# Optimization experiments

Measured on AMD Instinct MI355X. Metric: run time of the kernel, lower is better.

Reference implementation:

```python
import jax, jax.numpy as jnp
import numpy as np

N, E = 20000, 320000
H = 4            # heads per layer
C_IN, C_HID, C_OUT = 128, 64, 64
NEG_SLOPE = 0.2  # PyG GATConv default leaky_relu slope


def setup_inputs() -> dict:
    key = jax.random.key(0)
    ks = jax.random.split(key, 16)
    p = lambda k, shape: jax.random.normal(k, shape, jnp.float32) * 0.1
    return {
        "x": jax.random.normal(ks[0], (N, C_IN), jnp.float32),
        "edge_index": jax.random.randint(ks[1], (2, E), 0, N),
        # layer 0: in C_IN -> H*C_HID (concat)
        "W0": p(ks[2], (C_IN, H * C_HID)),
        "as0": p(ks[3], (H, C_HID)),
        "ad0": p(ks[4], (H, C_HID)),
        "b0": jnp.zeros((H * C_HID,), jnp.float32),
        # layer 1: in H*C_HID -> H*C_HID (concat)
        "W1": p(ks[5], (H * C_HID, H * C_HID)),
        "as1": p(ks[6], (H, C_HID)),
        "ad1": p(ks[7], (H, C_HID)),
        "b1": jnp.zeros((H * C_HID,), jnp.float32),
        # output layer: in H*C_HID -> C_OUT (mean over heads, concat=False)
        "W2": p(ks[8], (H * C_HID, H * C_OUT)),
        "as2": p(ks[9], (H, C_OUT)),
        "ad2": p(ks[10], (H, C_OUT)),
        "b2": jnp.zeros((C_OUT,), jnp.float32),
    }


def _gat_layer(x, src, dst, W, a_src, a_dst, b, concat):
    """PyG GATConv (eval mode): gather -> edge attention -> segment softmax -> scatter."""
    n = x.shape[0]
    h = (x @ W).reshape(n, H, -1)                      # [N, H, C]
    e_src = (h * a_src).sum(-1)                        # [N, H]
    e_dst = (h * a_dst).sum(-1)                        # [N, H]
    logits = jax.nn.leaky_relu(e_src[src] + e_dst[dst], NEG_SLOPE)   # [E', H]
    m = jax.lax.stop_gradient(jax.ops.segment_max(logits, dst, num_segments=n))
    ex = jnp.exp(logits - m[dst])
    denom = jax.ops.segment_sum(ex, dst, num_segments=n)
    alpha = ex / denom[dst]                            # [E', H] segment softmax per dst node
    out = jax.ops.segment_sum(h[src] * alpha[:, :, None], dst, num_segments=n)  # [N, H, C]
    out = out.reshape(n, -1) if concat else out.mean(axis=1)
    return out + b, alpha


def reference(x, edge_index, W0, as0, ad0, b0, W1, as1, ad1, b1, W2, as2, ad2, b2):
    n = x.shape[0]
    loops = jnp.arange(n, dtype=edge_index.dtype)      # GATConv adds self-loops
    src = jnp.concatenate([edge_index[0], loops])
    dst = jnp.concatenate([edge_index[1], loops])
    h, a0 = _gat_layer(x, src, dst, W0, as0, ad0, b0, True)
    h = jax.nn.elu(h)
    h, a1 = _gat_layer(h, src, dst, W1, as1, ad1, b1, True)
    h = jax.nn.elu(h)
    out, a2 = _gat_layer(h, src, dst, W2, as2, ad2, b2, False)
    return out, a0, a1, a2
```

## Files before the change

kernel.cpp:

```cpp
#include <hip/hip_runtime.h>
#include <hip/hip_bf16.h>
#include <math.h>

#define HCOLS 256
#define NHEAD 4
#define CDIM  64
#define NEG_SLOPE 0.2f

typedef __attribute__((ext_vector_type(8))) short bf16x8;
typedef __attribute__((ext_vector_type(4))) float f32x4;

__device__ __forceinline__ float leaky(float v) { return v > 0.f ? v : v * NEG_SLOPE; }
__device__ __forceinline__ unsigned short f2bf(float f) {
    unsigned u = __float_as_uint(f);
    u += 0x7fff + ((u >> 16) & 1);
    return (unsigned short)(u >> 16);
}

__device__ __forceinline__ void fma8(float* acc, uint4 hv, float a) {
    acc[0] = fmaf(a, __uint_as_float(hv.x << 16),          acc[0]);
    acc[1] = fmaf(a, __uint_as_float(hv.x & 0xffff0000u),  acc[1]);
    acc[2] = fmaf(a, __uint_as_float(hv.y << 16),          acc[2]);
    acc[3] = fmaf(a, __uint_as_float(hv.y & 0xffff0000u),  acc[3]);
    acc[4] = fmaf(a, __uint_as_float(hv.z << 16),          acc[4]);
    acc[5] = fmaf(a, __uint_as_float(hv.z & 0xffff0000u),  acc[5]);
    acc[6] = fmaf(a, __uint_as_float(hv.w << 16),          acc[6]);
    acc[7] = fmaf(a, __uint_as_float(hv.w & 0xffff0000u),  acc[7]);
}

__global__ void zero_deg_kernel(int* __restrict__ deg, int n) {
    int i = blockIdx.x * 256 + threadIdx.x;
    if (i < n) deg[i] = 0;
}

__global__ void deg_kernel(const int* __restrict__ ei, int* __restrict__ deg,
                           int E, int Ep) {
    int e = blockIdx.x * 256 + threadIdx.x;
    if (e >= Ep) return;
    int d = (e < E) ? ei[E + e] : (e - E);
    atomicAdd(&deg[d], 1);
}

__global__ void scan_kernel(const int* __restrict__ deg, int* __restrict__ rowptr,
                            int* __restrict__ cursor, int n) {
    __shared__ int wsum[16];
    int tid = threadIdx.x;
    int lane = tid & 63, w = tid >> 6;
    int CH = (n + 1023) >> 10;
    int base = tid * CH;
    int s = 0;
    for (int k = 0; k < CH; ++k) {
        int i = base + k;
        s += (i < n) ? deg[i] : 0;
    }
    int incl = s;
#pragma unroll
    for (int d = 1; d < 64; d <<= 1) {
        int t = __shfl_up(incl, d, 64);
        if (lane >= d) incl += t;
    }
    if (lane == 63) wsum[w] = incl;
    __syncthreads();
    if (w == 0) {
        int v = (lane < 16) ? wsum[lane] : 0;
#pragma unroll
        for (int d = 1; d < 16; d <<= 1) {
            int t = __shfl_up(v, d, 64);
            if (lane >= d) v += t;
        }
        if (lane < 16) wsum[lane] = v;
    }
    __syncthreads();
    int woff = (w == 0) ? 0 : wsum[w - 1];
    int run = woff + incl - s;
    for (int k = 0; k < CH; ++k) {
        int i = base + k;
        if (i < n) { rowptr[i] = run; cursor[i] = run; run += deg[i]; }
    }
    if (tid == 1023) rowptr[n] = run;
}

__global__ void fill_kernel(const int* __restrict__ ei, int* __restrict__ cursor,
                            int* __restrict__ eidx, int E, int Ep) {
    int e = blockIdx.x * 256 + threadIdx.x;
    if (e >= Ep) return;
    int d = (e < E) ? ei[E + e] : (e - E);
    int pos = atomicAdd(&cursor[d], 1);
    eidx[pos] = e;
}

__global__ void wconv_kernel(const float* __restrict__ W0, const float* __restrict__ W1,
                             const float* __restrict__ W2,
                             unsigned short* __restrict__ Wt0, unsigned short* __restrict__ Wt1,
                             unsigned short* __restrict__ Wt2) {
    __shared__ float t[32][33];
    int z = blockIdx.z;
    const float* W = (z == 0) ? W0 : (z == 1) ? W1 : W2;
    unsigned short* Wt = (z == 0) ? Wt0 : (z == 1) ? Wt1 : Wt2;
    int K = (z == 0) ? 128 : 256;
    if (blockIdx.y * 32 >= K) return;
    int bx = blockIdx.x;
    int by = blockIdx.y;
    int tx = threadIdx.x & 31, ty = threadIdx.x >> 5;
#pragma unroll
    for (int i = 0; i < 32; i += 8)
        t[ty + i][tx] = W[(by * 32 + ty + i) * HCOLS + bx * 32 + tx];
    __syncthreads();
#pragma unroll
    for (int i = 0; i < 32; i += 8)
        Wt[(size_t)(bx * 32 + ty + i) * K + by * 32 + tx] = f2bf(t[tx][ty + i]);
}

template <int K, bool SRC_F32>
__global__ void gemm_kernel(const void* __restrict__ Xv, const unsigned short* __restrict__ Wt,
                            unsigned short* __restrict__ Hout,
                            const float* __restrict__ As, const float* __restrict__ Ad,
                            float* __restrict__ esrc, float* __restrict__ edst,
                            int n) {
    constexpr int LDK = K + 16;
    __shared__ __align__(16) unsigned short a_sh[32 * LDK];
    int row0 = blockIdx.x * 32;
    int tid = threadIdx.x;

    constexpr int CH = 32 * K / 8;
    for (int c = tid; c < CH; c += 256) {
        int r = c / (K / 8), kc = c % (K / 8);
        int row = row0 + r;
        uint4 pack;
        if (row < n) {
            if (SRC_F32) {
                const float* X = (const float*)Xv;
                float4 f0 = *reinterpret_cast<const float4*>(&X[(size_t)row * K + kc * 8]);
                float4 f1 = *reinterpret_cast<const float4*>(&X[(size_t)row * K + kc * 8 + 4]);
                pack.x = f2bf(f0.x) | ((unsigned)f2bf(f0.y) << 16);
                pack.y = f2bf(f0.z) | ((unsigned)f2bf(f0.w) << 16);
                pack.z = f2bf(f1.x) | ((unsigned)f2bf(f1.y) << 16);
                pack.w = f2bf(f1.z) | ((unsigned)f2bf(f1.w) << 16);
            } else {
                const uint4* X = (const uint4*)Xv;
                pack = X[((size_t)row * K + kc * 8) / 8];
            }
        } else {
            pack = make_uint4(0, 0, 0, 0);
        }
        *reinterpret_cast<uint4*>(&a_sh[r * LDK + kc * 8]) = pack;
    }
    __syncthreads();

    int lane = tid & 63;
    int w = tid >> 6;
    int lr = lane & 15;
    int lk = (lane >> 4) * 8;

    f32x4 acc[2][4];
#pragma unroll
    for (int m = 0; m < 2; ++m)
#pragma unroll
        for (int nf = 0; nf < 4; ++nf) acc[m][nf] = (f32x4){0.f, 0.f, 0.f, 0.f};

    const unsigned short* wt = Wt + (size_t)(w * 64) * K;
#pragma unroll
    for (int ks = 0; ks < K / 32; ++ks) {
        bf16x8 a[2], b[4];
#pragma unroll
        for (int m = 0; m < 2; ++m)
            a[m] = *reinterpret_cast<const bf16x8*>(&a_sh[(16 * m + lr) * LDK + ks * 32 + lk]);
#pragma unroll
        for (int nf = 0; nf < 4; ++nf)
            b[nf] = *reinterpret_cast<const bf16x8*>(&wt[(size_t)(16 * nf + lr) * K + ks * 32 + lk]);
#pragma unroll
        for (int m = 0; m < 2; ++m)
#pragma unroll
            for (int nf = 0; nf < 4; ++nf)
                acc[m][nf] = __builtin_amdgcn_mfma_f32_16x16x32_bf16(a[m], b[nf], acc[m][nf], 0, 0, 0);
    }

    float as_v[4], ad_v[4];
#pragma unroll
    for (int nf = 0; nf < 4; ++nf) {
        as_v[nf] = As[w * 64 + 16 * nf + lr];
        ad_v[nf] = Ad[w * 64 + 16 * nf + lr];
    }
#pragma unroll
    for (int m = 0; m < 2; ++m) {
#pragma unroll
        for (int j = 0; j < 4; ++j) {
            int row_g = row0 + 16 * m + (lane >> 4) * 4 + j;
            bool ok = row_g < n;
#pragma unroll
            for (int nf = 0; nf < 4; ++nf) {
                if (ok) Hout[(size_t)row_g * HCOLS + w * 64 + 16 * nf + lr] = f2bf(acc[m][nf][j]);
            }
            float ps = acc[m][0][j] * as_v[0] + acc[m][1][j] * as_v[1] +
                       acc[m][2][j] * as_v[2] + acc[m][3][j] * as_v[3];
            float pd = acc[m][0][j] * ad_v[0] + acc[m][1][j] * ad_v[1] +
                       acc[m][2][j] * ad_v[2] + acc[m][3][j] * ad_v[3];
#pragma unroll
            for (int off = 1; off < 16; off <<= 1) {
                ps += __shfl_xor(ps, off, 64);
                pd += __shfl_xor(pd, off, 64);
            }
            if (lr == 0 && ok) {
                esrc[row_g * NHEAD + w] = ps;
                edst[row_g * NHEAD + w] = pd;
            }
        }
    }
}

template <int MODE>
__launch_bounds__(256, 4)
__global__ void attn_agg_kernel(const unsigned short* __restrict__ h,
                                const float* __restrict__ esrc,
                                const float* __restrict__ edst,
                                const int* __restrict__ ei,
                                const int* __restrict__ rowptr,
                                const int* __restrict__ eidx,
                                const float* __restrict__ bias,
                                float* __restrict__ alpha,
                                void* __restrict__ xout,
                                int n, int E) {
    __shared__ __align__(16) float aT[16][64][NHEAD];
    __shared__ int sArr[16][64];

    int tid = threadIdx.x;
    int wave = tid >> 6, lane = tid & 63;
    int g = lane >> 4, t = lane & 15;
    int nodeblk = blockIdx.x * 16;
    int nidx = wave * 4 + g;
    int node = nodeblk + nidx;
    bool gvalid = node < n;
    int s0 = 0, s1 = 0;
    if (gvalid) { s0 = rowptr[node]; s1 = rowptr[node + 1]; }
    int deg = s1 - s0;
    float4 ed = make_float4(0.f, 0.f, 0.f, 0.f);
    if (gvalid) ed = *reinterpret_cast<const float4*>(&edst[node * NHEAD]);

    const float NEGINF = -3.4e38f;
    float4 lgc[4]; int sc[4], ec[4];
    int degc = deg < 64 ? deg : 64;
    int nch = (degc + 15) >> 4;
    float4 mx = make_float4(NEGINF, NEGINF, NEGINF, NEGINF);
#pragma unroll
    for (int c = 0; c < 4; ++c) {
        sc[c] = 0; ec[c] = 0;
        lgc[c] = make_float4(NEGINF, NEGINF, NEGINF, NEGINF);
        if (c < nch) {
            int i = s0 + c * 16 + t;
            bool v = i < s1;
            int e = v ? eidx[i] : 0;
            int s = v ? ((e < E) ? ei[e] : (e - E)) : 0;
            sc[c] = s; ec[c] = e;
            if (v) {
                float4 es = *reinterpret_cast<const float4*>(&esrc[s * NHEAD]);
                lgc[c].x = leaky(es.x + ed.x);
                lgc[c].y = leaky(es.y + ed.y);
                lgc[c].z = leaky(es.z + ed.z);
                lgc[c].w = leaky(es.w + ed.w);
            }
            mx.x = fmaxf(mx.x, lgc[c].x);
            mx.y = fmaxf(mx.y, lgc[c].y);
            mx.z = fmaxf(mx.z, lgc[c].z);
            mx.w = fmaxf(mx.w, lgc[c].w);
        }
    }
    for (int i = s0 + 64 + t; i < s1; i += 16) {
        int e = eidx[i];
        int s = (e < E) ? ei[e] : (e - E);
        float4 es = *reinterpret_cast<const float4*>(&esrc[s * NHEAD]);
        mx.x = fmaxf(mx.x, leaky(es.x + ed.x));
        mx.y = fmaxf(mx.y, leaky(es.y + ed.y));
        mx.z = fmaxf(mx.z, leaky(es.z + ed.z));
        mx.w = fmaxf(mx.w, leaky(es.w + ed.w));
    }
#pragma unroll
    for (int off = 1; off < 16; off <<= 1) {
        mx.x = fmaxf(mx.x, __shfl_xor(mx.x, off, 64));
        mx.y = fmaxf(mx.y, __shfl_xor(mx.y, off, 64));
        mx.z = fmaxf(mx.z, __shfl_xor(mx.z, off, 64));
        mx.w = fmaxf(mx.w, __shfl_xor(mx.w, off, 64));
    }
    float4 exc[4];
    float4 sm = make_float4(0.f, 0.f, 0.f, 0.f);
#pragma unroll
    for (int c = 0; c < 4; ++c) {
        exc[c] = make_float4(0.f, 0.f, 0.f, 0.f);
        if (c < nch) {
            exc[c].x = __expf(lgc[c].x - mx.x);
            exc[c].y = __expf(lgc[c].y - mx.y);
            exc[c].z = __expf(lgc[c].z - mx.z);
            exc[c].w = __expf(lgc[c].w - mx.w);
            sm.x += exc[c].x; sm.y += exc[c].y; sm.z += exc[c].z; sm.w += exc[c].w;
        }
    }
    for (int i = s0 + 64 + t; i < s1; i += 16) {
        int e = eidx[i];
        int s = (e < E) ? ei[e] : (e - E);
        float4 es = *reinterpret_cast<const float4*>(&esrc[s * NHEAD]);
        sm.x += __expf(leaky(es.x + ed.x) - mx.x);
        sm.y += __expf(leaky(es.y + ed.y) - mx.y);
        sm.z += __expf(leaky(es.z + ed.z) - mx.z);
        sm.w += __expf(leaky(es.w + ed.w) - mx.w);
    }
#pragma unroll
    for (int off = 1; off < 16; off <<= 1) {
        sm.x += __shfl_xor(sm.x, off, 64);
        sm.y += __shfl_xor(sm.y, off, 64);
        sm.z += __shfl_xor(sm.z, off, 64);
        sm.w += __shfl_xor(sm.w, off, 64);
    }
    float4 inv = make_float4(1.f / sm.x, 1.f / sm.y, 1.f / sm.z, 1.f / sm.w);
#pragma unroll
    for (int c = 0; c < 4; ++c) {
        if (c < nch) {
            float4 al4;
            al4.x = exc[c].x * inv.x; al4.y = exc[c].y * inv.y;
            al4.z = exc[c].z * inv.z; al4.w = exc[c].w * inv.w;
            int i = s0 + c * 16 + t;
            if (i < s1) *reinterpret_cast<float4*>(&alpha[(size_t)ec[c] * NHEAD]) = al4;
            *reinterpret_cast<float4*>(&aT[nidx][c * 16 + t][0]) = al4;
            sArr[nidx][c * 16 + t] = sc[c];
        }
    }
    for (int i = s0 + 64 + t; i < s1; i += 16) {
        int e = eidx[i];
        int s = (e < E) ? ei[e] : (e - E);
        float4 es = *reinterpret_cast<const float4*>(&esrc[s * NHEAD]);
        float4 av;
        av.x = __expf(leaky(es.x + ed.x) - mx.x) * inv.x;
        av.y = __expf(leaky(es.y + ed.y) - mx.y) * inv.y;
        av.z = __expf(leaky(es.z + ed.z) - mx.z) * inv.z;
        av.w = __expf(leaky(es.w + ed.w) - mx.w) * inv.w;
        *reinterpret_cast<float4*>(&alpha[(size_t)e * NHEAD]) = av;
    }
    if (__any(deg > 64)) __threadfence();

    asm volatile("s_waitcnt lgkmcnt(0)" ::: "memory");
    __builtin_amdgcn_sched_barrier(0);

    int half = lane >> 5;
    int q = lane & 31;
    int head = q >> 3;
    unsigned byteoff = (unsigned)q * 16u;
    const char* hb = (const char*)h;

    for (int g2 = 0; g2 < 4; ++g2) {
        int nd = nodeblk + wave * 4 + g2;
        if (nd >= n) break;
        int t0 = rowptr[nd], t1 = rowptr[nd + 1];
        int dg = t1 - t0;
        int m = dg < 64 ? dg : 64;
        int m2 = (m + 1) & ~1;
        const float* ap = &aT[wave * 4 + g2][0][0] + head;
        const int* sp = &sArr[wave * 4 + g2][0];
        float acc[8];
#pragma unroll
        for (int k = 0; k < 8; ++k) acc[k] = 0.f;
        int j = 0;
        for (; j + 4 <= m2; j += 4) {
            int jA = j + half, jB = j + 2 + half;
            int sA = sp[jA], sB = sp[jB];
            float aA = ap[jA * NHEAD], aB = ap[jB * NHEAD];
            uint4 hA = *reinterpret_cast<const uint4*>(hb + (((unsigned)sA) << 9) + byteoff);
            uint4 hB = *reinterpret_cast<const uint4*>(hb + (((unsigned)sB) << 9) + byteoff);
            fma8(acc, hA, aA);
            fma8(acc, hB, aB);
        }
        for (; j < m2; j += 2) {
            int jA = j + half;
            int sA = sp[jA];
            float aA = ap[jA * NHEAD];
            uint4 hA = *reinterpret_cast<const uint4*>(hb + (((unsigned)sA) << 9) + byteoff);
            fma8(acc, hA, aA);
        }
        if (dg > 64) {
            for (int i = t0 + 64; i < t1; ++i) {
                if (half == 0) {
                    int e = eidx[i];
                    int s = (e < E) ? ei[e] : (e - E);
                    float a = alpha[(size_t)e * NHEAD + head];
                    uint4 hv = *reinterpret_cast<const uint4*>(hb + (((unsigned)s) << 9) + byteoff);
                    fma8(acc, hv, a);
                }
            }
        }
#pragma unroll
        for (int k = 0; k < 8; ++k) acc[k] += __shfl_xor(acc[k], 32, 64);

        if (MODE == 0) {
            if (half == 0) {
                float4 b0 = *reinterpret_cast<const float4*>(&bias[q * 8]);
                float4 b1 = *reinterpret_cast<const float4*>(&bias[q * 8 + 4]);
                float v0 = acc[0] + b0.x, v1 = acc[1] + b0.y, v2 = acc[2] + b0.z, v3 = acc[3] + b0.w;
                float v4 = acc[4] + b1.x, v5 = acc[5] + b1.y, v6 = acc[6] + b1.z, v7 = acc[7] + b1.w;
                v0 = v0 > 0.f ? v0 : expm1f(v0);
                v1 = v1 > 0.f ? v1 : expm1f(v1);
                v2 = v2 > 0.f ? v2 : expm1f(v2);
                v3 = v3 > 0.f ? v3 : expm1f(v3);
                v4 = v4 > 0.f ? v4 : expm1f(v4);
                v5 = v5 > 0.f ? v5 : expm1f(v5);
                v6 = v6 > 0.f ? v6 : expm1f(v6);
                v7 = v7 > 0.f ? v7 : expm1f(v7);
                uint4 o;
                o.x = (unsigned)f2bf(v0) | ((unsigned)f2bf(v1) << 16);
                o.y = (unsigned)f2bf(v2) | ((unsigned)f2bf(v3) << 16);
                o.z = (unsigned)f2bf(v4) | ((unsigned)f2bf(v5) << 16);
                o.w = (unsigned)f2bf(v6) | ((unsigned)f2bf(v7) << 16);
                *reinterpret_cast<uint4*>(&((unsigned short*)xout)[(size_t)nd * HCOLS + q * 8]) = o;
            }
        } else {
#pragma unroll
            for (int k = 0; k < 8; ++k) {
                acc[k] += __shfl_xor(acc[k], 8, 64);
                acc[k] += __shfl_xor(acc[k], 16, 64);
            }
            if (half == 0 && q < 8) {
                float* op = (float*)xout + (size_t)nd * CDIM + q * 8;
                float4 r0, r1;
                r0.x = acc[0] * 0.25f + bias[q * 8 + 0];
                r0.y = acc[1] * 0.25f + bias[q * 8 + 1];
                r0.z = acc[2] * 0.25f + bias[q * 8 + 2];
                r0.w = acc[3] * 0.25f + bias[q * 8 + 3];
                r1.x = acc[4] * 0.25f + bias[q * 8 + 4];
                r1.y = acc[5] * 0.25f + bias[q * 8 + 5];
                r1.z = acc[6] * 0.25f + bias[q * 8 + 6];
                r1.w = acc[7] * 0.25f + bias[q * 8 + 7];
                *reinterpret_cast<float4*>(op) = r0;
                *reinterpret_cast<float4*>(op + 4) = r1;
            }
        }
    }
}

extern "C" void kernel_launch(void* const* d_in, const int* in_sizes, int n_in,
                              void* d_out, int out_size, void* d_ws, size_t ws_size,
                              hipStream_t stream) {
    const float* x   = (const float*)d_in[0];
    const int*   ei  = (const int*)d_in[1];
    const float* W0  = (const float*)d_in[2];
    const float* as0 = (const float*)d_in[3];
    const float* ad0 = (const float*)d_in[4];
    const float* b0  = (const float*)d_in[5];
    const float* W1  = (const float*)d_in[6];
    const float* as1 = (const float*)d_in[7];
    const float* ad1 = (const float*)d_in[8];
    const float* b1  = (const float*)d_in[9];
    const float* W2  = (const float*)d_in[10];
    const float* as2 = (const float*)d_in[11];
    const float* ad2 = (const float*)d_in[12];
    const float* b2  = (const float*)d_in[13];

    const int N  = in_sizes[0] / 128;
    const int E  = in_sizes[1] / 2;
    const int Ep = E + N;

    float* out = (float*)d_out;
    float* a0  = out + (size_t)N * CDIM;
    float* a1  = a0 + (size_t)Ep * NHEAD;
    float* a2  = a1 + (size_t)Ep * NHEAD;

    char* wp = (char*)d_ws;
    auto carve = [&](size_t bytes) {
        char* p = wp;
        wp += (bytes + 255) & ~(size_t)255;
        return (void*)p;
    };
    unsigned short* hbuf = (unsigned short*)carve((size_t)N * HCOLS * 2);
    unsigned short* xbuf = (unsigned short*)carve((size_t)N * HCOLS * 2);
    float* esrc   = (float*)carve((size_t)N * NHEAD * 4);
    float* edst   = (float*)carve((size_t)N * NHEAD * 4);
    int*   deg    = (int*)carve((size_t)N * 4);
    int*   rowptr = (int*)carve((size_t)(N + 1) * 4);
    int*   cursor = (int*)carve((size_t)N * 4);
    int*   eidx   = (int*)carve((size_t)Ep * 4);
    unsigned short* Wt0 = (unsigned short*)carve((size_t)HCOLS * 128 * 2);
    unsigned short* Wt1 = (unsigned short*)carve((size_t)HCOLS * HCOLS * 2);
    unsigned short* Wt2 = (unsigned short*)carve((size_t)HCOLS * HCOLS * 2);

    zero_deg_kernel<<<(N + 255) / 256, 256, 0, stream>>>(deg, N);
    deg_kernel<<<(Ep + 255) / 256, 256, 0, stream>>>(ei, deg, E, Ep);
    scan_kernel<<<1, 1024, 0, stream>>>(deg, rowptr, cursor, N);
    fill_kernel<<<(Ep + 255) / 256, 256, 0, stream>>>(ei, cursor, eidx, E, Ep);

    wconv_kernel<<<dim3(8, 8, 3), 256, 0, stream>>>(W0, W1, W2, Wt0, Wt1, Wt2);

    int gemm_grid = (N + 31) / 32;
    int agg_grid  = (N + 15) / 16;

    gemm_kernel<128, true><<<gemm_grid, 256, 0, stream>>>(x, Wt0, hbuf, as0, ad0, esrc, edst, N);
    attn_agg_kernel<0><<<agg_grid, 256, 0, stream>>>(hbuf, esrc, edst, ei, rowptr, eidx, b0, a0, xbuf, N, E);

    gemm_kernel<256, false><<<gemm_grid, 256, 0, stream>>>(xbuf, Wt1, hbuf, as1, ad1, esrc, edst, N);
    attn_agg_kernel<0><<<agg_grid, 256, 0, stream>>>(hbuf, esrc, edst, ei, rowptr, eidx, b1, a1, xbuf, N, E);

    gemm_kernel<256, false><<<gemm_grid, 256, 0, stream>>>(xbuf, Wt2, hbuf, as2, ad2, esrc, edst, N);
    attn_agg_kernel<1><<<agg_grid, 256, 0, stream>>>(hbuf, esrc, edst, ei, rowptr, eidx, b2, a2, out, N, E);
}
```

Baseline: 233.5 us.

## Restructure aggregation to per-head edge-parallel loop and fuse prep kernels

The aggregation phase now loops over heads, with each wave lane group handling 8 edges in parallel per head (8 lanes covering a head's 64 channels). The shared alpha tile is stored head-major, and concat-mode outputs are staged in shared memory before a coalesced bias+ELU write. This is meant to raise memory-level parallelism on the gathered neighbor rows, at the cost of more cross-lane shuffle reductions and an extra shared buffer. Separately, the degree zeroing and weight transpose/convert kernels are merged into one launch to save a kernel launch.

```diff
diff --git a/kernel.cpp b/kernel.cpp
--- a/kernel.cpp
+++ b/kernel.cpp
@@ -28,9 +28,34 @@
     acc[7] = fmaf(a, __uint_as_float(hv.w & 0xffff0000u),  acc[7]);
 }
 
-__global__ void zero_deg_kernel(int* __restrict__ deg, int n) {
-    int i = blockIdx.x * 256 + threadIdx.x;
-    if (i < n) deg[i] = 0;
+__global__ void prep_kernel(const float* __restrict__ W0, const float* __restrict__ W1,
+                            const float* __restrict__ W2,
+                            unsigned short* __restrict__ Wt0, unsigned short* __restrict__ Wt1,
+                            unsigned short* __restrict__ Wt2,
+                            int* __restrict__ deg, int n, int nzb) {
+    int b = blockIdx.x;
+    if (b < nzb) {
+        int i = b * 256 + threadIdx.x;
+        if (i < n) deg[i] = 0;
+        return;
+    }
+    b -= nzb;
+    int z = b >> 6;
+    int rem = b & 63;
+    int bx = rem & 7, by = rem >> 3;
+    const float* W = (z == 0) ? W0 : (z == 1) ? W1 : W2;
+    unsigned short* Wt = (z == 0) ? Wt0 : (z == 1) ? Wt1 : Wt2;
+    int K = (z == 0) ? 128 : 256;
+    if (by * 32 >= K) return;
+    __shared__ float t[32][33];
+    int tx = threadIdx.x & 31, ty = threadIdx.x >> 5;
+#pragma unroll
+    for (int i = 0; i < 32; i += 8)
+        t[ty + i][tx] = W[(by * 32 + ty + i) * HCOLS + bx * 32 + tx];
+    __syncthreads();
+#pragma unroll
+    for (int i = 0; i < 32; i += 8)
+        Wt[(size_t)(bx * 32 + ty + i) * K + by * 32 + tx] = f2bf(t[tx][ty + i]);
 }
 
 __global__ void deg_kernel(const int* __restrict__ ei, int* __restrict__ deg,
@@ -87,28 +112,6 @@
     int d = (e < E) ? ei[E + e] : (e - E);
     int pos = atomicAdd(&cursor[d], 1);
     eidx[pos] = e;
-}
-
-__global__ void wconv_kernel(const float* __restrict__ W0, const float* __restrict__ W1,
-                             const float* __restrict__ W2,
-                             unsigned short* __restrict__ Wt0, unsigned short* __restrict__ Wt1,
-                             unsigned short* __restrict__ Wt2) {
-    __shared__ float t[32][33];
-    int z = blockIdx.z;
-    const float* W = (z == 0) ? W0 : (z == 1) ? W1 : W2;
-    unsigned short* Wt = (z == 0) ? Wt0 : (z == 1) ? Wt1 : Wt2;
-    int K = (z == 0) ? 128 : 256;
-    if (blockIdx.y * 32 >= K) return;
-    int bx = blockIdx.x;
-    int by = blockIdx.y;
-    int tx = threadIdx.x & 31, ty = threadIdx.x >> 5;
-#pragma unroll
-    for (int i = 0; i < 32; i += 8)
-        t[ty + i][tx] = W[(by * 32 + ty + i) * HCOLS + bx * 32 + tx];
-    __syncthreads();
-#pragma unroll
-    for (int i = 0; i < 32; i += 8)
-        Wt[(size_t)(bx * 32 + ty + i) * K + by * 32 + tx] = f2bf(t[tx][ty + i]);
 }
 
 template <int K, bool SRC_F32>
@@ -220,8 +223,9 @@
                                 float* __restrict__ alpha,
                                 void* __restrict__ xout,
                                 int n, int E) {
-    __shared__ __align__(16) float aT[16][64][NHEAD];
+    __shared__ __align__(16) float aTh[16][NHEAD][72];
     __shared__ int sArr[16][64];
+    __shared__ __align__(16) float outbuf[MODE == 0 ? 16 : 1][MODE == 0 ? 256 : 4];
 
     int tid = threadIdx.x;
     int wave = tid >> 6, lane = tid & 63;
@@ -318,8 +322,12 @@
             al4.z = exc[c].z * inv.z; al4.w = exc[c].w * inv.w;
             int i = s0 + c * 16 + t;
             if (i < s1) *reinterpret_cast<float4*>(&alpha[(size_t)ec[c] * NHEAD]) = al4;
-            *reinterpret_cast<float4*>(&aT[nidx][c * 16 + t][0]) = al4;
-            sArr[nidx][c * 16 + t] = sc[c];
+            int eo = c * 16 + t;
+            aTh[nidx][0][eo] = al4.x;
+            aTh[nidx][1][eo] = al4.y;
+            aTh[nidx][2][eo] = al4.z;
+            aTh[nidx][3][eo] = al4.w;
+            sArr[nidx][eo] = sc[c];
         }
     }
     for (int i = s0 + 64 + t; i < s1; i += 16) {
@@ -338,94 +346,116 @@
     asm volatile("s_waitcnt lgkmcnt(0)" ::: "memory");
     __builtin_amdgcn_sched_barrier(0);
 
-    int half = lane >> 5;
-    int q = lane & 31;
-    int head = q >> 3;
-    unsigned byteoff = (unsigned)q * 16u;
+    int ed8 = lane >> 3;
+    int ch  = lane & 7;
     const char* hb = (const char*)h;
-
+    unsigned chb = (unsigned)(ch * 16);
+
+    int t0r[4], t1r[4];
+#pragma unroll
     for (int g2 = 0; g2 < 4; ++g2) {
         int nd = nodeblk + wave * 4 + g2;
-        if (nd >= n) break;
-        int t0 = rowptr[nd], t1 = rowptr[nd + 1];
-        int dg = t1 - t0;
-        int m = dg < 64 ? dg : 64;
-        int m2 = (m + 1) & ~1;
-        const float* ap = &aT[wave * 4 + g2][0][0] + head;
-        const int* sp = &sArr[wave * 4 + g2][0];
-        float acc[8];
-#pragma unroll
-        for (int k = 0; k < 8; ++k) acc[k] = 0.f;
-        int j = 0;
-        for (; j + 4 <= m2; j += 4) {
-            int jA = j + half, jB = j + 2 + half;
-            int sA = sp[jA], sB = sp[jB];
-            float aA = ap[jA * NHEAD], aB = ap[jB * NHEAD];
-            uint4 hA = *reinterpret_cast<const uint4*>(hb + (((unsigned)sA) << 9) + byteoff);
-            uint4 hB = *reinterpret_cast<const uint4*>(hb + (((unsigned)sB) << 9) + byteoff);
-            fma8(acc, hA, aA);
-            fma8(acc, hB, aB);
-        }
-        for (; j < m2; j += 2) {
-            int jA = j + half;
-            int sA = sp[jA];
-            float aA = ap[jA * NHEAD];
-            uint4 hA = *reinterpret_cast<const uint4*>(hb + (((unsigned)sA) << 9) + byteoff);
-            fma8(acc, hA, aA);
-        }
-        if (dg > 64) {
-            for (int i = t0 + 64; i < t1; ++i) {
-                if (half == 0) {
-                    int e = eidx[i];
-                    int s = (e < E) ? ei[e] : (e - E);
-                    float a = alpha[(size_t)e * NHEAD + head];
-                    uint4 hv = *reinterpret_cast<const uint4*>(hb + (((unsigned)s) << 9) + byteoff);
-                    fma8(acc, hv, a);
+        t0r[g2] = 0; t1r[g2] = 0;
+        if (nd < n) { t0r[g2] = rowptr[nd]; t1r[g2] = rowptr[nd + 1]; }
+    }
+
+    float macc[4][8];
+    if (MODE == 1) {
+#pragma unroll
+        for (int g2 = 0; g2 < 4; ++g2)
+#pragma unroll
+            for (int k = 0; k < 8; ++k) macc[g2][k] = 0.f;
+    }
+
+#pragma unroll 1
+    for (int hd = 0; hd < NHEAD; ++hd) {
+        unsigned hoff = (unsigned)(hd * 128) + chb;
+#pragma unroll
+        for (int g2 = 0; g2 < 4; ++g2) {
+            int nd = nodeblk + wave * 4 + g2;
+            if (nd >= n) continue;
+            int dg = t1r[g2] - t0r[g2];
+            int m = dg < 64 ? dg : 64;
+            const float* ap = &aTh[wave * 4 + g2][hd][0];
+            const int*   sp = &sArr[wave * 4 + g2][0];
+            float acc[8];
+#pragma unroll
+            for (int k = 0; k < 8; ++k) acc[k] = 0.f;
+            for (int j = 0; j < m; j += 8) {
+                int e = j + ed8;
+                int s = sp[e];
+                float a = ap[e];
+                uint4 hv = *reinterpret_cast<const uint4*>(hb + (((unsigned)s) << 9) + hoff);
+                fma8(acc, hv, a);
+            }
+            if (dg > 64) {
+                for (int i = t0r[g2] + 64; i < t1r[g2]; ++i) {
+                    int e2 = eidx[i];
+                    int s = (e2 < E) ? ei[e2] : (e2 - E);
+                    float a = alpha[(size_t)e2 * NHEAD + hd];
+                    if (ed8 == 0) {
+                        uint4 hv = *reinterpret_cast<const uint4*>(hb + (((unsigned)s) << 9) + hoff);
+                        fma8(acc, hv, a);
+                    }
                 }
             }
-        }
-#pragma unroll
-        for (int k = 0; k < 8; ++k) acc[k] += __shfl_xor(acc[k], 32, 64);
-
-        if (MODE == 0) {
-            if (half == 0) {
-                float4 b0 = *reinterpret_cast<const float4*>(&bias[q * 8]);
-                float4 b1 = *reinterpret_cast<const float4*>(&bias[q * 8 + 4]);
-                float v0 = acc[0] + b0.x, v1 = acc[1] + b0.y, v2 = acc[2] + b0.z, v3 = acc[3] + b0.w;
-                float v4 = acc[4] + b1.x, v5 = acc[5] + b1.y, v6 = acc[6] + b1.z, v7 = acc[7] + b1.w;
-                v0 = v0 > 0.f ? v0 : expm1f(v0);
-                v1 = v1 > 0.f ? v1 : expm1f(v1);
-                v2 = v2 > 0.f ? v2 : expm1f(v2);
-                v3 = v3 > 0.f ? v3 : expm1f(v3);
-                v4 = v4 > 0.f ? v4 : expm1f(v4);
-                v5 = v5 > 0.f ? v5 : expm1f(v5);
-                v6 = v6 > 0.f ? v6 : expm1f(v6);
-                v7 = v7 > 0.f ? v7 : expm1f(v7);
-                uint4 o;
-                o.x = (unsigned)f2bf(v0) | ((unsigned)f2bf(v1) << 16);
-                o.y = (unsigned)f2bf(v2) | ((unsigned)f2bf(v3) << 16);
-                o.z = (unsigned)f2bf(v4) | ((unsigned)f2bf(v5) << 16);
-                o.w = (unsigned)f2bf(v6) | ((unsigned)f2bf(v7) << 16);
-                *reinterpret_cast<uint4*>(&((unsigned short*)xout)[(size_t)nd * HCOLS + q * 8]) = o;
-            }
-        } else {
 #pragma unroll
             for (int k = 0; k < 8; ++k) {
                 acc[k] += __shfl_xor(acc[k], 8, 64);
                 acc[k] += __shfl_xor(acc[k], 16, 64);
-            }
-            if (half == 0 && q < 8) {
-                float* op = (float*)xout + (size_t)nd * CDIM + q * 8;
+                acc[k] += __shfl_xor(acc[k], 32, 64);
+            }
+            if (MODE == 0) {
+                if (ed8 == 0) {
+                    float4 w0 = make_float4(acc[0], acc[1], acc[2], acc[3]);
+                    float4 w1 = make_float4(acc[4], acc[5], acc[6], acc[7]);
+                    *reinterpret_cast<float4*>(&outbuf[wave * 4 + g2][hd * 64 + ch * 8])     = w0;
+                    *reinterpret_cast<float4*>(&outbuf[wave * 4 + g2][hd * 64 + ch * 8 + 4]) = w1;
+                }
+            } else {
+#pragma unroll
+                for (int k = 0; k < 8; ++k) macc[g2][k] += acc[k];
+            }
+        }
+    }
+
+    if (MODE == 0) {
+        asm volatile("s_waitcnt lgkmcnt(0)" ::: "memory");
+        __builtin_amdgcn_sched_barrier(0);
+        float4 bv = *reinterpret_cast<const float4*>(&bias[lane * 4]);
+#pragma unroll
+        for (int g2 = 0; g2 < 4; ++g2) {
+            int nd = nodeblk + wave * 4 + g2;
+            if (nd >= n) continue;
+            float4 v = *reinterpret_cast<const float4*>(&outbuf[wave * 4 + g2][lane * 4]);
+            v.x += bv.x; v.y += bv.y; v.z += bv.z; v.w += bv.w;
+            v.x = v.x > 0.f ? v.x : expm1f(v.x);
+            v.y = v.y > 0.f ? v.y : expm1f(v.y);
+            v.z = v.z > 0.f ? v.z : expm1f(v.z);
+            v.w = v.w > 0.f ? v.w : expm1f(v.w);
+            ushort4 o;
+            o.x = f2bf(v.x); o.y = f2bf(v.y); o.z = f2bf(v.z); o.w = f2bf(v.w);
+            *reinterpret_cast<ushort4*>(&((unsigned short*)xout)[(size_t)nd * HCOLS + lane * 4]) = o;
+        }
+    } else {
+        if (ed8 == 0) {
+            float4 b0 = *reinterpret_cast<const float4*>(&bias[ch * 8]);
+            float4 b1 = *reinterpret_cast<const float4*>(&bias[ch * 8 + 4]);
+#pragma unroll
+            for (int g2 = 0; g2 < 4; ++g2) {
+                int nd = nodeblk + wave * 4 + g2;
+                if (nd >= n) continue;
+                float* op = (float*)xout + (size_t)nd * CDIM + ch * 8;
                 float4 r0, r1;
-                r0.x = acc[0] * 0.25f + bias[q * 8 + 0];
-                r0.y = acc[1] * 0.25f + bias[q * 8 + 1];
-                r0.z = acc[2] * 0.25f + bias[q * 8 + 2];
-                r0.w = acc[3] * 0.25f + bias[q * 8 + 3];
-                r1.x = acc[4] * 0.25f + bias[q * 8 + 4];
-                r1.y = acc[5] * 0.25f + bias[q * 8 + 5];
-                r1.z = acc[6] * 0.25f + bias[q * 8 + 6];
-                r1.w = acc[7] * 0.25f + bias[q * 8 + 7];
-                *reinterpret_cast<float4*>(op) = r0;
+                r0.x = macc[g2][0] * 0.25f + b0.x;
+                r0.y = macc[g2][1] * 0.25f + b0.y;
+                r0.z = macc[g2][2] * 0.25f + b0.z;
+                r0.w = macc[g2][3] * 0.25f + b0.w;
+                r1.x = macc[g2][4] * 0.25f + b1.x;
+                r1.y = macc[g2][5] * 0.25f + b1.y;
+                r1.z = macc[g2][6] * 0.25f + b1.z;
+                r1.w = macc[g2][7] * 0.25f + b1.w;
+                *reinterpret_cast<float4*>(op)     = r0;
                 *reinterpret_cast<float4*>(op + 4) = r1;
             }
         }
@@ -477,13 +507,12 @@
     unsigned short* Wt1 = (unsigned short*)carve((size_t)HCOLS * HCOLS * 2);
     unsigned short* Wt2 = (unsigned short*)carve((size_t)HCOLS * HCOLS * 2);
 
-    zero_deg_kernel<<<(N + 255) / 256, 256, 0, stream>>>(deg, N);
+    int nzb = (N + 255) / 256;
+    prep_kernel<<<nzb + 192, 256, 0, stream>>>(W0, W1, W2, Wt0, Wt1, Wt2, deg, N, nzb);
     deg_kernel<<<(Ep + 255) / 256, 256, 0, stream>>>(ei, deg, E, Ep);
     scan_kernel<<<1, 1024, 0, stream>>>(deg, rowptr, cursor, N);
     fill_kernel<<<(Ep + 255) / 256, 256, 0, stream>>>(ei, cursor, eidx, E, Ep);
 
-    wconv_kernel<<<dim3(8, 8, 3), 256, 0, stream>>>(W0, W1, W2, Wt0, Wt1, Wt2);
-
     int gemm_grid = (N + 31) / 32;
     int agg_grid  = (N + 15) / 16;
 
```

New measurement: 307.0 us. 1.31x slower.

## Fuse attention aggregation with next layer's GEMM and merge prep kernels

Applied to the files above, without the earlier changes.

The attention-aggregate kernel for layers 0 and 1 now writes its ELU'd bf16 node features into shared memory and immediately runs the next layer's MFMA GEMM and attention-logit projection on those 16 rows. This removes the xbuf round trip through global memory and two kernel launches. Double-buffered h/esrc/edst arrays avoid read-after-write hazards across blocks. The deg zeroing and weight conversion kernels are merged into one launch. In exchange, each block reads the full weight matrix from global/L2 for only 16 rows, and shared memory use per block goes up.

```diff
diff --git a/kernel.cpp b/kernel.cpp
--- a/kernel.cpp
+++ b/kernel.cpp
@@ -28,9 +28,34 @@
     acc[7] = fmaf(a, __uint_as_float(hv.w & 0xffff0000u),  acc[7]);
 }
 
-__global__ void zero_deg_kernel(int* __restrict__ deg, int n) {
-    int i = blockIdx.x * 256 + threadIdx.x;
-    if (i < n) deg[i] = 0;
+__global__ void prep_kernel(const float* __restrict__ W0, const float* __restrict__ W1,
+                            const float* __restrict__ W2,
+                            unsigned short* __restrict__ Wt0, unsigned short* __restrict__ Wt1,
+                            unsigned short* __restrict__ Wt2,
+                            int* __restrict__ deg, int n, int nzb) {
+    int b = blockIdx.x;
+    if (b < nzb) {
+        int i = b * 256 + threadIdx.x;
+        if (i < n) deg[i] = 0;
+        return;
+    }
+    b -= nzb;
+    int z = b >> 6;
+    int rem = b & 63;
+    int bx = rem & 7, by = rem >> 3;
+    const float* W = (z == 0) ? W0 : (z == 1) ? W1 : W2;
+    unsigned short* Wt = (z == 0) ? Wt0 : (z == 1) ? Wt1 : Wt2;
+    int K = (z == 0) ? 128 : 256;
+    if (by * 32 >= K) return;
+    __shared__ float t[32][33];
+    int tx = threadIdx.x & 31, ty = threadIdx.x >> 5;
+#pragma unroll
+    for (int i = 0; i < 32; i += 8)
+        t[ty + i][tx] = W[(by * 32 + ty + i) * HCOLS + bx * 32 + tx];
+    __syncthreads();
+#pragma unroll
+    for (int i = 0; i < 32; i += 8)
+        Wt[(size_t)(bx * 32 + ty + i) * K + by * 32 + tx] = f2bf(t[tx][ty + i]);
 }
 
 __global__ void deg_kernel(const int* __restrict__ ei, int* __restrict__ deg,
@@ -87,28 +112,6 @@
     int d = (e < E) ? ei[E + e] : (e - E);
     int pos = atomicAdd(&cursor[d], 1);
     eidx[pos] = e;
-}
-
-__global__ void wconv_kernel(const float* __restrict__ W0, const float* __restrict__ W1,
-                             const float* __restrict__ W2,
-                             unsigned short* __restrict__ Wt0, unsigned short* __restrict__ Wt1,
-                             unsigned short* __restrict__ Wt2) {
-    __shared__ float t[32][33];
-    int z = blockIdx.z;
-    const float* W = (z == 0) ? W0 : (z == 1) ? W1 : W2;
-    unsigned short* Wt = (z == 0) ? Wt0 : (z == 1) ? Wt1 : Wt2;
-    int K = (z == 0) ? 128 : 256;
-    if (blockIdx.y * 32 >= K) return;
-    int bx = blockIdx.x;
-    int by = blockIdx.y;
-    int tx = threadIdx.x & 31, ty = threadIdx.x >> 5;
-#pragma unroll
-    for (int i = 0; i < 32; i += 8)
-        t[ty + i][tx] = W[(by * 32 + ty + i) * HCOLS + bx * 32 + tx];
-    __syncthreads();
-#pragma unroll
-    for (int i = 0; i < 32; i += 8)
-        Wt[(size_t)(bx * 32 + ty + i) * K + by * 32 + tx] = f2bf(t[tx][ty + i]);
 }
 
 template <int K, bool SRC_F32>
@@ -208,25 +211,18 @@
     }
 }
 
-template <int MODE>
-__launch_bounds__(256, 4)
-__global__ void attn_agg_kernel(const unsigned short* __restrict__ h,
-                                const float* __restrict__ esrc,
-                                const float* __restrict__ edst,
-                                const int* __restrict__ ei,
-                                const int* __restrict__ rowptr,
-                                const int* __restrict__ eidx,
-                                const float* __restrict__ bias,
-                                float* __restrict__ alpha,
-                                void* __restrict__ xout,
-                                int n, int E) {
-    __shared__ __align__(16) float aT[16][64][NHEAD];
-    __shared__ int sArr[16][64];
-
+template <int LDX>
+__device__ __forceinline__ void attn_phaseAB(
+        const unsigned short* __restrict__ h,
+        const float* __restrict__ esrc, const float* __restrict__ edst,
+        const int* __restrict__ ei, const int* __restrict__ rowptr,
+        const int* __restrict__ eidx, const float* __restrict__ bias,
+        float* __restrict__ alpha,
+        float (*aT)[64][NHEAD], int (*sArr)[64], unsigned short (*xs)[LDX],
+        int nodeblk, int n, int E) {
     int tid = threadIdx.x;
     int wave = tid >> 6, lane = tid & 63;
     int g = lane >> 4, t = lane & 15;
-    int nodeblk = blockIdx.x * 16;
     int nidx = wave * 4 + g;
     int node = nodeblk + nidx;
     bool gvalid = node < n;
@@ -345,14 +341,15 @@
     const char* hb = (const char*)h;
 
     for (int g2 = 0; g2 < 4; ++g2) {
-        int nd = nodeblk + wave * 4 + g2;
-        if (nd >= n) break;
+        int nl = wave * 4 + g2;
+        int nd = nodeblk + nl;
+        if (nd >= n) continue;
         int t0 = rowptr[nd], t1 = rowptr[nd + 1];
         int dg = t1 - t0;
         int m = dg < 64 ? dg : 64;
         int m2 = (m + 1) & ~1;
-        const float* ap = &aT[wave * 4 + g2][0][0] + head;
-        const int* sp = &sArr[wave * 4 + g2][0];
+        const float* ap = &aT[nl][0][0] + head;
+        const int* sp = &sArr[nl][0];
         float acc[8];
 #pragma unroll
         for (int k = 0; k < 8; ++k) acc[k] = 0.f;
@@ -387,47 +384,303 @@
 #pragma unroll
         for (int k = 0; k < 8; ++k) acc[k] += __shfl_xor(acc[k], 32, 64);
 
-        if (MODE == 0) {
-            if (half == 0) {
-                float4 b0 = *reinterpret_cast<const float4*>(&bias[q * 8]);
-                float4 b1 = *reinterpret_cast<const float4*>(&bias[q * 8 + 4]);
-                float v0 = acc[0] + b0.x, v1 = acc[1] + b0.y, v2 = acc[2] + b0.z, v3 = acc[3] + b0.w;
-                float v4 = acc[4] + b1.x, v5 = acc[5] + b1.y, v6 = acc[6] + b1.z, v7 = acc[7] + b1.w;
-                v0 = v0 > 0.f ? v0 : expm1f(v0);
-                v1 = v1 > 0.f ? v1 : expm1f(v1);
-                v2 = v2 > 0.f ? v2 : expm1f(v2);
-                v3 = v3 > 0.f ? v3 : expm1f(v3);
-                v4 = v4 > 0.f ? v4 : expm1f(v4);
-                v5 = v5 > 0.f ? v5 : expm1f(v5);
-                v6 = v6 > 0.f ? v6 : expm1f(v6);
-                v7 = v7 > 0.f ? v7 : expm1f(v7);
-                uint4 o;
-                o.x = (unsigned)f2bf(v0) | ((unsigned)f2bf(v1) << 16);
-                o.y = (unsigned)f2bf(v2) | ((unsigned)f2bf(v3) << 16);
-                o.z = (unsigned)f2bf(v4) | ((unsigned)f2bf(v5) << 16);
-                o.w = (unsigned)f2bf(v6) | ((unsigned)f2bf(v7) << 16);
-                *reinterpret_cast<uint4*>(&((unsigned short*)xout)[(size_t)nd * HCOLS + q * 8]) = o;
+        if (half == 0) {
+            float4 b0 = *reinterpret_cast<const float4*>(&bias[q * 8]);
+            float4 b1 = *reinterpret_cast<const float4*>(&bias[q * 8 + 4]);
+            float v0 = acc[0] + b0.x, v1 = acc[1] + b0.y, v2 = acc[2] + b0.z, v3 = acc[3] + b0.w;
+            float v4 = acc[4] + b1.x, v5 = acc[5] + b1.y, v6 = acc[6] + b1.z, v7 = acc[7] + b1.w;
+            v0 = v0 > 0.f ? v0 : expm1f(v0);
+            v1 = v1 > 0.f ? v1 : expm1f(v1);
+            v2 = v2 > 0.f ? v2 : expm1f(v2);
+            v3 = v3 > 0.f ? v3 : expm1f(v3);
+            v4 = v4 > 0.f ? v4 : expm1f(v4);
+            v5 = v5 > 0.f ? v5 : expm1f(v5);
+            v6 = v6 > 0.f ? v6 : expm1f(v6);
+            v7 = v7 > 0.f ? v7 : expm1f(v7);
+            uint4 o;
+            o.x = (unsigned)f2bf(v0) | ((unsigned)f2bf(v1) << 16);
+            o.y = (unsigned)f2bf(v2) | ((unsigned)f2bf(v3) << 16);
+            o.z = (unsigned)f2bf(v4) | ((unsigned)f2bf(v5) << 16);
+            o.w = (unsigned)f2bf(v6) | ((unsigned)f2bf(v7) << 16);
+            *reinterpret_cast<uint4*>(&xs[nl][q * 8]) = o;
+        }
+    }
+}
+
+__launch_bounds__(256, 4)
+__global__ void attn_gemm_kernel(const unsigned short* __restrict__ h_in,
+                                 const float* __restrict__ esrc_in,
+                                 const float* __restrict__ edst_in,
+                                 const int* __restrict__ ei,
+                                 const int* __restrict__ rowptr,
+                                 const int* __restrict__ eidx,
+                                 const float* __restrict__ bias,
+                                 float* __restrict__ alpha,
+                                 const unsigned short* __restrict__ Wt,
+                                 unsigned short* __restrict__ Hout,
+                                 const float* __restrict__ As, const float* __restrict__ Ad,
+                                 float* __restrict__ esrc_out, float* __restrict__ edst_out,
+                                 int n, int E) {
+    constexpr int K = 256;
+    constexpr int LDX = K + 16;
+    __shared__ __align__(16) float aT[16][64][NHEAD];
+    __shared__ int sArr[16][64];
+    __shared__ __align__(16) unsigned short xs[16][LDX];
+
+    int nodeblk = blockIdx.x * 16;
+    attn_phaseAB<LDX>(h_in, esrc_in, edst_in, ei, rowptr, eidx, bias, alpha,
+                      aT, sArr, xs, nodeblk, n, E);
+    __syncthreads();
+
+    int tid = threadIdx.x;
+    int lane = tid & 63;
+    int w = tid >> 6;
+    int lr = lane & 15;
+    int lk = (lane >> 4) * 8;
+
+    f32x4 acc[4];
+#pragma unroll
+    for (int nf = 0; nf < 4; ++nf) acc[nf] = (f32x4){0.f, 0.f, 0.f, 0.f};
+
+    const unsigned short* wt = Wt + (size_t)(w * 64) * K;
+#pragma unroll
+    for (int ks = 0; ks < K / 32; ++ks) {
+        bf16x8 a = *reinterpret_cast<const bf16x8*>(&xs[lr][ks * 32 + lk]);
+        bf16x8 b[4];
+#pragma unroll
+        for (int nf = 0; nf < 4; ++nf)
+            b[nf] = *reinterpret_cast<const bf16x8*>(&wt[(size_t)(16 * nf + lr) * K + ks * 32 + lk]);
+#pragma unroll
+        for (int nf = 0; nf < 4; ++nf)
+            acc[nf] = __builtin_amdgcn_mfma_f32_16x16x32_bf16(a, b[nf], acc[nf], 0, 0, 0);
+    }
+
+    float as_v[4], ad_v[4];
+#pragma unroll
+    for (int nf = 0; nf < 4; ++nf) {
+        as_v[nf] = As[w * 64 + 16 * nf + lr];
+        ad_v[nf] = Ad[w * 64 + 16 * nf + lr];
+    }
+#pragma unroll
+    for (int j = 0; j < 4; ++j) {
+        int row_g = nodeblk + (lane >> 4) * 4 + j;
+        bool ok = row_g < n;
+#pragma unroll
+        for (int nf = 0; nf < 4; ++nf) {
+            if (ok) Hout[(size_t)row_g * HCOLS + w * 64 + 16 * nf + lr] = f2bf(acc[nf][j]);
+        }
+        float ps = acc[0][j] * as_v[0] + acc[1][j] * as_v[1] +
+                   acc[2][j] * as_v[2] + acc[3][j] * as_v[3];
+        float pd = acc[0][j] * ad_v[0] + acc[1][j] * ad_v[1] +
+                   acc[2][j] * ad_v[2] + acc[3][j] * ad_v[3];
+#pragma unroll
+        for (int off = 1; off < 16; off <<= 1) {
+            ps += __shfl_xor(ps, off, 64);
+            pd += __shfl_xor(pd, off, 64);
+        }
+        if (lr == 0 && ok) {
+            esrc_out[row_g * NHEAD + w] = ps;
+            edst_out[row_g * NHEAD + w] = pd;
+        }
+    }
+}
+
+__launch_bounds__(256, 4)
+__global__ void attn_mean_kernel(const unsigned short* __restrict__ h,
+                                 const float* __restrict__ esrc,
+                                 const float* __restrict__ edst,
+                                 const int* __restrict__ ei,
+                                 const int* __restrict__ rowptr,
+                                 const int* __restrict__ eidx,
+                                 const float* __restrict__ bias,
+                                 float* __restrict__ alpha,
+                                 float* __restrict__ xout,
+                                 int n, int E) {
+    __shared__ __align__(16) float aT[16][64][NHEAD];
+    __shared__ int sArr[16][64];
+
+    int tid = threadIdx.x;
+    int wave = tid >> 6, lane = tid & 63;
+    int g = lane >> 4, t = lane & 15;
+    int nodeblk = blockIdx.x * 16;
+    int nidx = wave * 4 + g;
+    int node = nodeblk + nidx;
+    bool gvalid = node < n;
+    int s0 = 0, s1 = 0;
+    if (gvalid) { s0 = rowptr[node]; s1 = rowptr[node + 1]; }
+    int deg = s1 - s0;
+    float4 ed = make_float4(0.f, 0.f, 0.f, 0.f);
+    if (gvalid) ed = *reinterpret_cast<const float4*>(&edst[node * NHEAD]);
+
+    const float NEGINF = -3.4e38f;
+    float4 lgc[4]; int sc[4], ec[4];
+    int degc = deg < 64 ? deg : 64;
+    int nch = (degc + 15) >> 4;
+    float4 mx = make_float4(NEGINF, NEGINF, NEGINF, NEGINF);
+#pragma unroll
+    for (int c = 0; c < 4; ++c) {
+        sc[c] = 0; ec[c] = 0;
+        lgc[c] = make_float4(NEGINF, NEGINF, NEGINF, NEGINF);
+        if (c < nch) {
+            int i = s0 + c * 16 + t;
+            bool v = i < s1;
+            int e = v ? eidx[i] : 0;
+            int s = v ? ((e < E) ? ei[e] : (e - E)) : 0;
+            sc[c] = s; ec[c] = e;
+            if (v) {
+                float4 es = *reinterpret_cast<const float4*>(&esrc[s * NHEAD]);
+                lgc[c].x = leaky(es.x + ed.x);
+                lgc[c].y = leaky(es.y + ed.y);
+                lgc[c].z = leaky(es.z + ed.z);
+                lgc[c].w = leaky(es.w + ed.w);
             }
-        } else {
-#pragma unroll
-            for (int k = 0; k < 8; ++k) {
-                acc[k] += __shfl_xor(acc[k], 8, 64);
-                acc[k] += __shfl_xor(acc[k], 16, 64);
+            mx.x = fmaxf(mx.x, lgc[c].x);
+            mx.y = fmaxf(mx.y, lgc[c].y);
+            mx.z = fmaxf(mx.z, lgc[c].z);
+            mx.w = fmaxf(mx.w, lgc[c].w);
+        }
+    }
+    for (int i = s0 + 64 + t; i < s1; i += 16) {
+        int e = eidx[i];
+        int s = (e < E) ? ei[e] : (e - E);
+        float4 es = *reinterpret_cast<const float4*>(&esrc[s * NHEAD]);
+        mx.x = fmaxf(mx.x, leaky(es.x + ed.x));
+        mx.y = fmaxf(mx.y, leaky(es.y + ed.y));
+        mx.z = fmaxf(mx.z, leaky(es.z + ed.z));
+        mx.w = fmaxf(mx.w, leaky(es.w + ed.w));
+    }
+#pragma unroll
+    for (int off = 1; off < 16; off <<= 1) {
+        mx.x = fmaxf(mx.x, __shfl_xor(mx.x, off, 64));
+        mx.y = fmaxf(mx.y, __shfl_xor(mx.y, off, 64));
+        mx.z = fmaxf(mx.z, __shfl_xor(mx.z, off, 64));
+        mx.w = fmaxf(mx.w, __shfl_xor(mx.w, off, 64));
+    }
+    float4 exc[4];
+    float4 sm = make_float4(0.f, 0.f, 0.f, 0.f);
+#pragma unroll
+    for (int c = 0; c < 4; ++c) {
+        exc[c] = make_float4(0.f, 0.f, 0.f, 0.f);
+        if (c < nch) {
+            exc[c].x = __expf(lgc[c].x - mx.x);
+            exc[c].y = __expf(lgc[c].y - mx.y);
+            exc[c].z = __expf(lgc[c].z - mx.z);
+            exc[c].w = __expf(lgc[c].w - mx.w);
+            sm.x += exc[c].x; sm.y += exc[c].y; sm.z += exc[c].z; sm.w += exc[c].w;
+        }
+    }
+    for (int i = s0 + 64 + t; i < s1; i += 16) {
+        int e = eidx[i];
+        int s = (e < E) ? ei[e] : (e - E);
+        float4 es = *reinterpret_cast<const float4*>(&esrc[s * NHEAD]);
+        sm.x += __expf(leaky(es.x + ed.x) - mx.x);
+        sm.y += __expf(leaky(es.y + ed.y) - mx.y);
+        sm.z += __expf(leaky(es.z + ed.z) - mx.z);
+        sm.w += __expf(leaky(es.w + ed.w) - mx.w);
+    }
+#pragma unroll
+    for (int off = 1; off < 16; off <<= 1) {
+        sm.x += __shfl_xor(sm.x, off, 64);
+        sm.y += __shfl_xor(sm.y, off, 64);
+        sm.z += __shfl_xor(sm.z, off, 64);
+        sm.w += __shfl_xor(sm.w, off, 64);
+    }
+    float4 inv = make_float4(1.f / sm.x, 1.f / sm.y, 1.f / sm.z, 1.f / sm.w);
+#pragma unroll
+    for (int c = 0; c < 4; ++c) {
+        if (c < nch) {
+            float4 al4;
+            al4.x = exc[c].x * inv.x; al4.y = exc[c].y * inv.y;
+            al4.z = exc[c].z * inv.z; al4.w = exc[c].w * inv.w;
+            int i = s0 + c * 16 + t;
+            if (i < s1) *reinterpret_cast<float4*>(&alpha[(size_t)ec[c] * NHEAD]) = al4;
+            int eo = c * 16 + t;
+            *reinterpret_cast<float4*>(&aT[nidx][eo][0]) = al4;
+            sArr[nidx][eo] = sc[c];
+        }
+    }
+    for (int i = s0 + 64 + t; i < s1; i += 16) {
+        int e = eidx[i];
+        int s = (e < E) ? ei[e] : (e - E);
+        float4 es = *reinterpret_cast<const float4*>(&esrc[s * NHEAD]);
+        float4 av;
+        av.x = __expf(leaky(es.x + ed.x) - mx.x) * inv.x;
+        av.y = __expf(leaky(es.y + ed.y) - mx.y) * inv.y;
+        av.z = __expf(leaky(es.z + ed.z) - mx.z) * inv.z;
+        av.w = __expf(leaky(es.w + ed.w) - mx.w) * inv.w;
+        *reinterpret_cast<float4*>(&alpha[(size_t)e * NHEAD]) = av;
+    }
+    if (__any(deg > 64)) __threadfence();
+
+    asm volatile("s_waitcnt lgkmcnt(0)" ::: "memory");
+    __builtin_amdgcn_sched_barrier(0);
+
+    int half = lane >> 5;
+    int q = lane & 31;
+    int head = q >> 3;
+    unsigned byteoff = (unsigned)q * 16u;
+    const char* hb = (const char*)h;
+
+    for (int g2 = 0; g2 < 4; ++g2) {
+        int nl = wave * 4 + g2;
+        int nd = nodeblk + nl;
+        if (nd >= n) continue;
+        int t0 = rowptr[nd], t1 = rowptr[nd + 1];
+        int dg = t1 - t0;
+        int m = dg < 64 ? dg : 64;
+        int m2 = (m + 1) & ~1;
+        const float* ap = &aT[nl][0][0] + head;
+        const int* sp = &sArr[nl][0];
+        float acc[8];
+#pragma unroll
+        for (int k = 0; k < 8; ++k) acc[k] = 0.f;
+        int j = 0;
+        for (; j + 4 <= m2; j += 4) {
+            int jA = j + half, jB = j + 2 + half;
+            int sA = sp[jA], sB = sp[jB];
+            float aA = ap[jA * NHEAD], aB = ap[jB * NHEAD];
+            uint4 hA = *reinterpret_cast<const uint4*>(hb + (((unsigned)sA) << 9) + byteoff);
+            uint4 hB = *reinterpret_cast<const uint4*>(hb + (((unsigned)sB) << 9) + byteoff);
+            fma8(acc, hA, aA);
+            fma8(acc, hB, aB);
+        }
+        for (; j < m2; j += 2) {
+            int jA = j + half;
+            int sA = sp[jA];
+            float aA = ap[jA * NHEAD];
+            uint4 hA = *reinterpret_cast<const uint4*>(hb + (((unsigned)sA) << 9) + byteoff);
+            fma8(acc, hA, aA);
+        }
+        if (dg > 64) {
+            for (int i = t0 + 64; i < t1; ++i) {
+                if (half == 0) {
+                    int e = eidx[i];
+                    int s = (e < E) ? ei[e] : (e - E);
+                    float a = alpha[(size_t)e * NHEAD + head];
+                    uint4 hv = *reinterpret_cast<const uint4*>(hb + (((unsigned)s) << 9) + byteoff);
+                    fma8(acc, hv, a);
+                }
             }
-            if (half == 0 && q < 8) {
-                float* op = (float*)xout + (size_t)nd * CDIM + q * 8;
-                float4 r0, r1;
-                r0.x = acc[0] * 0.25f + bias[q * 8 + 0];
-                r0.y = acc[1] * 0.25f + bias[q * 8 + 1];
-                r0.z = acc[2] * 0.25f + bias[q * 8 + 2];
-                r0.w = acc[3] * 0.25f + bias[q * 8 + 3];
-                r1.x = acc[4] * 0.25f + bias[q * 8 + 4];
-                r1.y = acc[5] * 0.25f + bias[q * 8 + 5];
-                r1.z = acc[6] * 0.25f + bias[q * 8 + 6];
-                r1.w = acc[7] * 0.25f + bias[q * 8 + 7];
-                *reinterpret_cast<float4*>(op) = r0;
-                *reinterpret_cast<float4*>(op + 4) = r1;
-            }
+        }
+#pragma unroll
+        for (int k = 0; k < 8; ++k) {
+            acc[k] += __shfl_xor(acc[k], 32, 64);
+            acc[k] += __shfl_xor(acc[k], 8, 64);
+            acc[k] += __shfl_xor(acc[k], 16, 64);
+        }
+        if (half == 0 && q < 8) {
+            float* op = xout + (size_t)nd * CDIM + q * 8;
+            float4 r0, r1;
+            r0.x = acc[0] * 0.25f + bias[q * 8 + 0];
+            r0.y = acc[1] * 0.25f + bias[q * 8 + 1];
+            r0.z = acc[2] * 0.25f + bias[q * 8 + 2];
+            r0.w = acc[3] * 0.25f + bias[q * 8 + 3];
+            r1.x = acc[4] * 0.25f + bias[q * 8 + 4];
+            r1.y = acc[5] * 0.25f + bias[q * 8 + 5];
+            r1.z = acc[6] * 0.25f + bias[q * 8 + 6];
+            r1.w = acc[7] * 0.25f + bias[q * 8 + 7];
+            *reinterpret_cast<float4*>(op)     = r0;
+            *reinterpret_cast<float4*>(op + 4) = r1;
         }
     }
 }
@@ -465,10 +718,12 @@
         wp += (bytes + 255) & ~(size_t)255;
         return (void*)p;
     };
-    unsigned short* hbuf = (unsigned short*)carve((size_t)N * HCOLS * 2);
-    unsigned short* xbuf = (unsigned short*)carve((size_t)N * HCOLS * 2);
-    float* esrc   = (float*)carve((size_t)N * NHEAD * 4);
-    float* edst   = (float*)carve((size_t)N * NHEAD * 4);
+    unsigned short* hbufA = (unsigned short*)carve((size_t)N * HCOLS * 2);
+    unsigned short* hbufB = (unsigned short*)carve((size_t)N * HCOLS * 2);
+    float* esrcA  = (float*)carve((size_t)N * NHEAD * 4);
+    float* edstA  = (float*)carve((size_t)N * NHEAD * 4);
+    float* esrcB  = (float*)carve((size_t)N * NHEAD * 4);
+    float* edstB  = (float*)carve((size_t)N * NHEAD * 4);
     int*   deg    = (int*)carve((size_t)N * 4);
     int*   rowptr = (int*)carve((size_t)(N + 1) * 4);
     int*   cursor = (int*)carve((size_t)N * 4);
@@ -477,22 +732,20 @@
     unsigned short* Wt1 = (unsigned short*)carve((size_t)HCOLS * HCOLS * 2);
     unsigned short* Wt2 = (unsigned short*)carve((size_t)HCOLS * HCOLS * 2);
 
-    zero_deg_kernel<<<(N + 255) / 256, 256, 0, stream>>>(deg, N);
+    int nzb = (N + 255) / 256;
+    prep_kernel<<<nzb + 192, 256, 0, stream>>>(W0, W1, W2, Wt0, Wt1, Wt2, deg, N, nzb);
     deg_kernel<<<(Ep + 255) / 256, 256, 0, stream>>>(ei, deg, E, Ep);
     scan_kernel<<<1, 1024, 0, stream>>>(deg, rowptr, cursor, N);
     fill_kernel<<<(Ep + 255) / 256, 256, 0, stream>>>(ei, cursor, eidx, E, Ep);
 
-    wconv_kernel<<<dim3(8, 8, 3), 256, 0, stream>>>(W0, W1, W2, Wt0, Wt1, Wt2);
-
     int gemm_grid = (N + 31) / 32;
     int agg_grid  = (N + 15) / 16;
 
-    gemm_kernel<128, true><<<gemm_grid, 256, 0, stream>>>(x, Wt0, hbuf, as0, ad0, esrc, edst, N);
-    attn_agg_kernel<0><<<agg_grid, 256, 0, stream>>>(hbuf, esrc, edst, ei, rowptr, eidx, b0, a0, xbuf, N, E);
-
-    gemm_kernel<256, false><<<gemm_grid, 256, 0, stream>>>(xbuf, Wt1, hbuf, as1, ad1, esrc, edst, N);
-    attn_agg_kernel<0><<<agg_grid, 256, 0, stream>>>(hbuf, esrc, edst, ei, rowptr, eidx, b1, a1, xbuf, N, E);
-
-    gemm_kernel<256, false><<<gemm_grid, 256, 0, stream>>>(xbuf, Wt2, hbuf, as2, ad2, esrc, edst, N);
-    attn_agg_kernel<1><<<agg_grid, 256, 0, stream>>>(hbuf, esrc, edst, ei, rowptr, eidx, b2, a2, out, N, E);
-}
+    gemm_kernel<128, true><<<gemm_grid, 256, 0, stream>>>(x, Wt0, hbufA, as0, ad0, esrcA, edstA, N);
+    attn_gemm_kernel<<<agg_grid, 256, 0, stream>>>(hbufA, esrcA, edstA, ei, rowptr, eidx,
+                                                   b0, a0, Wt1, hbufB, as1, ad1, esrcB, edstB, N, E);
+    attn_gemm_kernel<<<agg_grid, 256, 0, stream>>>(hbufB, esrcB, edstB, ei, rowptr, eidx,
+                                                   b1, a1, Wt2, hbufA, as2, ad2, esrcA, edstA, N, E);
+    attn_mean_kernel<<<agg_grid, 256, 0, stream>>>(hbufA, esrcA, edstA, ei, rowptr, eidx,
+                                                   b2, a2, out, N, E);
+}
```

New measurement: 218.6 us. 6.4% less time.
